# Kernel tuning notes

Hardware: AMD Instinct MI355X
Metric: run time of the kernel (lower is better)

The kernel has to match this reference:

```python
import jax, jax.numpy as jnp
import numpy as np

N = 20000      # num nodes
E = 320000     # num edges (avg degree 16)
F_IN = 518     # object_feature_dim
D = 128        # node_embedding_dim (= GAT out_channels)
ED = 32        # edge_embedding_dim
R = 26         # num_relations
H = 4          # GAT heads (concat=False -> mean over heads)
HID = 256      # node_encoder hidden


def _gat_layer(x, src, dst, ea, lin, lin_e, att_s, att_d, att_e, bias):
    """PyG GATConv: add_self_loops=True (fill_value='mean'), concat=False, negative_slope=0.2."""
    n = x.shape[0]
    ones = jnp.ones((src.shape[0],), x.dtype)
    cnt = jax.ops.segment_sum(ones, dst, num_segments=n)                    # [N]
    loop_ea = jax.ops.segment_sum(ea, dst, num_segments=n) / jnp.maximum(cnt, 1.0)[:, None]
    idx = jnp.arange(n)
    s = jnp.concatenate([src, idx])
    d = jnp.concatenate([dst, idx])
    ea2 = jnp.concatenate([ea, loop_ea], axis=0)                            # [E+N, ED]
    h = (x @ lin).reshape(n, H, D)                                          # [N,H,D]
    a_s = jnp.einsum('nhd,hd->nh', h, att_s)                                # [N,H]
    a_d = jnp.einsum('nhd,hd->nh', h, att_d)
    e = (ea2 @ lin_e).reshape(-1, H, D)                                     # [E+N,H,D]
    a_e = jnp.einsum('ehd,hd->eh', e, att_e)
    alpha = jax.nn.leaky_relu(a_s[s] + a_d[d] + a_e, 0.2)                   # [E+N,H]
    amax = jax.ops.segment_max(alpha, d, num_segments=n)
    alpha = jnp.exp(alpha - amax[d])
    denom = jax.ops.segment_sum(alpha, d, num_segments=n)
    alpha = alpha / (denom[d] + 1e-16)                                      # segment softmax
    msg = h[s] * alpha[:, :, None]                                          # [E+N,H,D]
    out = jax.ops.segment_sum(msg, d, num_segments=n)                       # [N,H,D]
    return out.mean(axis=1) + bias                                          # concat=False


def setup_inputs() -> dict:
    key = jax.random.key(0)
    ks = jax.random.split(key, 18)
    g = lambda k, shp, s=0.05: jax.random.normal(k, shp, jnp.float32) * s
    return {
        'x': g(ks[0], (N, F_IN), 1.0),
        'edge_index': jax.random.randint(ks[1], (2, E), 0, N),
        'edge_type': jax.random.randint(ks[2], (E,), 0, R),
        'w1': g(ks[3], (F_IN, HID)), 'b1': jnp.zeros((HID,), jnp.float32),
        'w2': g(ks[4], (HID, D)),    'b2': jnp.zeros((D,), jnp.float32),
        'rel_emb': g(ks[5], (R, ED), 1.0),
        'lin1': g(ks[6], (D, H * D)), 'line1': g(ks[7], (ED, H * D)),
        'atts1': g(ks[8], (H, D)), 'attd1': g(ks[9], (H, D)), 'atte1': g(ks[10], (H, D)),
        'bias1': jnp.zeros((D,), jnp.float32),
        'lin2': g(ks[11], (D, H * D)), 'line2': g(ks[12], (ED, H * D)),
        'atts2': g(ks[13], (H, D)), 'attd2': g(ks[14], (H, D)), 'atte2': g(ks[15], (H, D)),
        'bias2': jnp.zeros((D,), jnp.float32),
    }


def reference(x, edge_index, edge_type, w1, b1, w2, b2, rel_emb,
              lin1, line1, atts1, attd1, atte1, bias1,
              lin2, line2, atts2, attd2, atte2, bias2):
    src, dst = edge_index[0], edge_index[1]
    # node encoder (dropout inactive in eval)
    h = jax.nn.relu(x @ w1 + b1) @ w2 + b2                                  # [N,D]
    ea = rel_emb[edge_type]                                                 # [E,ED]
    h = jax.nn.relu(_gat_layer(h, src, dst, ea, lin1, line1, atts1, attd1, atte1, bias1))
    h = jax.nn.relu(_gat_layer(h, src, dst, ea, lin2, line2, atts2, attd2, atte2, bias2))
    return h
```

## Files before the change

### kernel.cpp

```cpp
#include <hip/hip_runtime.h>
#include <math.h>

#define N_NODES 20000
#define MP      20032
#define N_EDGES 320000
#define F_IN    518
#define HIDDEN  256
#define DIM     128
#define NH      4

typedef __attribute__((ext_vector_type(8))) short bf16x8;
typedef __attribute__((ext_vector_type(4))) float f32x4;
typedef unsigned short ushort_t;

__device__ __forceinline__ float lrelu02(float x) { return x > 0.f ? x : 0.2f * x; }

__device__ __forceinline__ void gl_lds16(const void* g, void* l) {
    __builtin_amdgcn_global_load_lds(
        (const __attribute__((address_space(1))) unsigned int*)g,
        (__attribute__((address_space(3))) unsigned int*)l, 16, 0, 0);
}

__device__ __forceinline__ unsigned int hi16(float v) { return __float_as_uint(v) >> 16; }
__device__ __forceinline__ unsigned int lo16(float v) {
    unsigned int h = __float_as_uint(v) & 0xFFFF0000u;
    return __float_as_uint(v - __uint_as_float(h)) >> 16;
}
__device__ __forceinline__ unsigned int rnd16(float v) {
    unsigned int u = __float_as_uint(v);
    return (u + 0x7FFFu + ((u >> 16) & 1u)) >> 16;
}
__device__ __forceinline__ float bfl(unsigned int u) { return __uint_as_float(u << 16); }
__device__ __forceinline__ float bfh(unsigned int u) { return __uint_as_float(u & 0xFFFF0000u); }

__global__ __launch_bounds__(256, 4) void gemm_mfma_v2(
    const ushort_t* __restrict__ Ah, const ushort_t* __restrict__ Al,
    const ushort_t* __restrict__ Bh, const ushort_t* __restrict__ Bl,
    const float* __restrict__ bias,
    int M, int K8, int N, int act,
    float* __restrict__ Cf,
    ushort_t* __restrict__ Ch, ushort_t* __restrict__ Cl,
    ushort_t* __restrict__ Cb,
    ushort_t* __restrict__ Ca)
{
    __shared__ __align__(16) ushort_t lds[12288];
    const int tid = threadIdx.x;
    const int w = tid >> 6, lane = tid & 63;
    const int row0 = blockIdx.y * 64, col0 = blockIdx.x * 128;
    const int nkb = K8 >> 2;
    const int m16 = lane & 15, q = lane >> 4;
    const bool use_al = (Al != nullptr);

    f32x4 acc[4][2] = {};

    for (int kb = 0; kb < nkb; ++kb) {
        const size_t kc = (size_t)(kb * 4 + w);
        const size_t aoff = (kc * MP + row0) * 8 + lane * 8;
        const size_t boff = (kc * N + col0) * 8 + lane * 8;
        gl_lds16(Ah + aoff, &lds[w * 512]);
        if (use_al) gl_lds16(Al + aoff, &lds[2048 + w * 512]);
        gl_lds16(Bh + boff,       &lds[4096 + w * 1024]);
        gl_lds16(Bh + boff + 512, &lds[4096 + w * 1024 + 512]);
        gl_lds16(Bl + boff,       &lds[8192 + w * 1024]);
        gl_lds16(Bl + boff + 512, &lds[8192 + w * 1024 + 512]);
        __syncthreads();

        bf16x8 fah[4], fal[4], fbh[2], fbl[2];
        const int fa = q * 512 + m16 * 8;
        #pragma unroll
        for (int mi = 0; mi < 4; ++mi) {
            fah[mi] = *(const bf16x8*)&lds[fa + mi * 128];
            if (use_al) fal[mi] = *(const bf16x8*)&lds[2048 + fa + mi * 128];
        }
        const int fb = q * 1024 + (w * 32 + m16) * 8;
        #pragma unroll
        for (int ni = 0; ni < 2; ++ni) {
            fbh[ni] = *(const bf16x8*)&lds[4096 + fb + ni * 128];
            fbl[ni] = *(const bf16x8*)&lds[8192 + fb + ni * 128];
        }
        #pragma unroll
        for (int mi = 0; mi < 4; ++mi)
            #pragma unroll
            for (int ni = 0; ni < 2; ++ni) {
                acc[mi][ni] = __builtin_amdgcn_mfma_f32_16x16x32_bf16(fah[mi], fbh[ni], acc[mi][ni], 0, 0, 0);
                acc[mi][ni] = __builtin_amdgcn_mfma_f32_16x16x32_bf16(fah[mi], fbl[ni], acc[mi][ni], 0, 0, 0);
            }
        if (use_al) {
            #pragma unroll
            for (int mi = 0; mi < 4; ++mi)
                #pragma unroll
                for (int ni = 0; ni < 2; ++ni)
                    acc[mi][ni] = __builtin_amdgcn_mfma_f32_16x16x32_bf16(fal[mi], fbh[ni], acc[mi][ni], 0, 0, 0);
        }
        __syncthreads();
    }

    #pragma unroll
    for (int ni = 0; ni < 2; ++ni) {
        const int col = col0 + w * 32 + ni * 16 + m16;
        const float bb = bias ? bias[col] : 0.f;
        #pragma unroll
        for (int mi = 0; mi < 4; ++mi) {
            #pragma unroll
            for (int r = 0; r < 4; ++r) {
                const int row = row0 + mi * 16 + q * 4 + r;
                if (row < M) {
                    float v = acc[mi][ni][r] + bb;
                    if (act) v = fmaxf(v, 0.f);
                    if (Cf) Cf[(size_t)row * N + col] = v;
                    if (Cb) Cb[(size_t)row * N + col] = (ushort_t)rnd16(v);
                    const size_t p = (((size_t)(col >> 3)) * MP + row) * 8 + (col & 7);
                    if (Ch) { Ch[p] = (ushort_t)hi16(v); Cl[p] = (ushort_t)lo16(v); }
                    if (Ca) Ca[p] = (ushort_t)rnd16(v);
                }
            }
        }
    }
}

__global__ __launch_bounds__(256) void conv_a_t_kernel(
    const float* __restrict__ x, ushort_t* __restrict__ xh, ushort_t* __restrict__ xl)
{
    __shared__ float tile[64][68];
    const int tid = threadIdx.x;
    const int r0 = blockIdx.x * 64;
    const int c0 = blockIdx.y * 64;

    #pragma unroll
    for (int it = 0; it < 4; ++it) {
        const int r = (tid >> 4) + it * 16;
        const int c = (tid & 15) * 4;
        const int gr = r0 + r, gc = c0 + c;
        float4 v = {0.f, 0.f, 0.f, 0.f};
        if (gr < N_NODES) {
            if (gc + 3 < F_IN) {
                v = *(const float4*)(x + (size_t)gr * F_IN + gc);
            } else {
                float tmp[4] = {0.f, 0.f, 0.f, 0.f};
                #pragma unroll
                for (int u = 0; u < 4; ++u)
                    if (gc + u < F_IN) tmp[u] = x[(size_t)gr * F_IN + gc + u];
                v.x = tmp[0]; v.y = tmp[1]; v.z = tmp[2]; v.w = tmp[3];
            }
        }
        tile[r][c] = v.x; tile[r][c+1] = v.y; tile[r][c+2] = v.z; tile[r][c+3] = v.w;
    }
    __syncthreads();

    const int k8l = tid >> 5;
    const int k8 = (c0 >> 3) + k8l;
    if (k8 >= 68) return;
    const int rr = (tid & 31) * 2;
    #pragma unroll
    for (int u = 0; u < 2; ++u) {
        const int r = rr + u;
        unsigned int hp[4], lp[4];
        #pragma unroll
        for (int i = 0; i < 4; ++i) {
            const float v0 = tile[r][k8l * 8 + 2 * i];
            const float v1 = tile[r][k8l * 8 + 2 * i + 1];
            hp[i] = (hi16(v1) << 16) | hi16(v0);
            lp[i] = (lo16(v1) << 16) | lo16(v0);
        }
        const size_t p = ((size_t)k8 * MP + r0 + r) * 8;
        *(uint4*)(xh + p) = make_uint4(hp[0], hp[1], hp[2], hp[3]);
        *(uint4*)(xl + p) = make_uint4(lp[0], lp[1], lp[2], lp[3]);
    }
}

#define W1_T (68 * 256 * 8)
#define W2_T (32 * 128 * 8)
#define L_T  (16 * 512 * 8)
__global__ __launch_bounds__(256) void conv_w_all_kernel(
    const float* __restrict__ w1, const float* __restrict__ w2,
    const float* __restrict__ l0, const float* __restrict__ l1,
    ushort_t* __restrict__ w1h, ushort_t* __restrict__ w1l,
    ushort_t* __restrict__ w2h, ushort_t* __restrict__ w2l,
    ushort_t* __restrict__ l0h, ushort_t* __restrict__ l0l,
    ushort_t* __restrict__ l1h, ushort_t* __restrict__ l1l)
{
    int idx = blockIdx.x * 256 + threadIdx.x;
    const float* w; ushort_t *bh, *bl; int K, N, local;
    if (idx < W1_T) { w = w1; bh = w1h; bl = w1l; K = F_IN; N = HIDDEN; local = idx; }
    else if (idx < W1_T + W2_T) { w = w2; bh = w2h; bl = w2l; K = HIDDEN; N = DIM; local = idx - W1_T; }
    else if (idx < W1_T + W2_T + L_T) { w = l0; bh = l0h; bl = l0l; K = DIM; N = 512; local = idx - W1_T - W2_T; }
    else if (idx < W1_T + W2_T + 2 * L_T) { w = l1; bh = l1h; bl = l1l; K = DIM; N = 512; local = idx - W1_T - W2_T - L_T; }
    else return;
    const int j = local & 7;
    const int rem = local >> 3;
    const int n = rem % N;
    const int k = (rem / N) * 8 + j;
    const float v = (k < K) ? w[(size_t)k * N + n] : 0.f;
    bh[local] = (ushort_t)hi16(v);
    bl[local] = (ushort_t)lo16(v);
}

__global__ __launch_bounds__(256) void wa2_kernel(
    const float* __restrict__ lin0, const float* __restrict__ lin1,
    const float* __restrict__ atts0, const float* __restrict__ attd0,
    const float* __restrict__ atts1, const float* __restrict__ attd1,
    float* __restrict__ wa_s0, float* __restrict__ wa_d0,
    float* __restrict__ wa_s1, float* __restrict__ wa_d1)
{
    const int wrk = blockIdx.x * 256 + threadIdx.x;
    if (wrk >= 2048) return;
    const int L = wrk >> 10;
    const int sd = (wrk >> 9) & 1;
    const int p = wrk & 511;
    const int h = p >> 7, d = p & 127;
    const float* lin = L ? lin1 : lin0;
    const float* av = L ? (sd ? attd1 : atts1) : (sd ? attd0 : atts0);
    float* out = L ? (sd ? wa_d1 : wa_s1) : (sd ? wa_d0 : wa_s0);
    const float* lp = lin + (size_t)d * (NH * DIM) + h * DIM;
    const float* ap = av + h * DIM;
    float acc = 0.f;
    #pragma unroll 8
    for (int i = 0; i < DIM; ++i) acc += lp[i] * ap[i];
    out[h * DIM + d] = acc;
}

__global__ __launch_bounds__(256) void as_ad_kernel(
    const float* __restrict__ xb, const float* __restrict__ wa_s,
    const float* __restrict__ wa_d, float* __restrict__ a_s, float* __restrict__ a_d)
{
    const int gw = blockIdx.x * 4 + (threadIdx.x >> 6);
    const int lane = threadIdx.x & 63;
    if (gw >= N_NODES * NH) return;
    const int n = gw >> 2, h = gw & 3;
    const float* hp = xb + (size_t)n * DIM;
    float2 hv = *(const float2*)(hp + lane * 2);
    float2 sv = *(const float2*)(wa_s + h * DIM + lane * 2);
    float2 dv = *(const float2*)(wa_d + h * DIM + lane * 2);
    float s = hv.x * sv.x + hv.y * sv.y;
    float d = hv.x * dv.x + hv.y * dv.y;
    #pragma unroll
    for (int off = 32; off > 0; off >>= 1) {
        s += __shfl_down(s, off);
        d += __shfl_down(d, off);
    }
    if (lane == 0) { a_s[n * 4 + h] = s; a_d[n * 4 + h] = d; }
}

__global__ __launch_bounds__(128) void rel_table2_kernel(
    const float* __restrict__ rel_emb,
    const float* __restrict__ line0, const float* __restrict__ atte0,
    const float* __restrict__ line1, const float* __restrict__ atte1,
    float* __restrict__ table)
{
    __shared__ float we[32][NH];
    const int L = blockIdx.x;
    const float* line = L ? line1 : line0;
    const float* atte = L ? atte1 : atte0;
    float* tab = table + L * 128;
    const int tid = threadIdx.x;
    const int k = tid >> 2, h = tid & 3;
    float acc = 0.f;
    for (int d = 0; d < DIM; ++d)
        acc += line[(size_t)k * (NH * DIM) + h * DIM + d] * atte[h * DIM + d];
    we[k][h] = acc;
    __syncthreads();
    if (tid < 26 * NH) {
        int r = tid >> 2, hh = tid & 3;
        float t = 0.f;
        for (int kk = 0; kk < 32; ++kk) t += rel_emb[r * 32 + kk] * we[kk][hh];
        tab[r * 4 + hh] = t;
    }
}

__global__ __launch_bounds__(256) void hist_kernel(
    const int* __restrict__ dst, int* __restrict__ cnt)
{
    const int e = blockIdx.x * blockDim.x + threadIdx.x;
    if (e >= N_EDGES) return;
    atomicAdd(&cnt[dst[e]], 1);
}

__global__ __launch_bounds__(1024) void scan_kernel(
    const int* __restrict__ cnt, int* __restrict__ ptr, int* __restrict__ ptr_copy)
{
    __shared__ int tsum[1024];
    const int tid = threadIdx.x;
    const int CH = 20;
    const int base = tid * CH;
    int s = 0;
    #pragma unroll
    for (int i = 0; i < CH; ++i) {
        int idx = base + i;
        if (idx < N_NODES) s += cnt[idx];
    }
    tsum[tid] = s;
    __syncthreads();
    for (int off = 1; off < 1024; off <<= 1) {
        int v = (tid >= off) ? tsum[tid - off] : 0;
        __syncthreads();
        tsum[tid] += v;
        __syncthreads();
    }
    int run = (tid == 0) ? 0 : tsum[tid - 1];
    #pragma unroll
    for (int i = 0; i < CH; ++i) {
        int idx = base + i;
        if (idx < N_NODES) {
            ptr[idx] = run;
            ptr_copy[idx] = run;
            run += cnt[idx];
        }
    }
    if (tid == 0) ptr[N_NODES] = N_EDGES;
}

__global__ __launch_bounds__(256) void scatter_kernel(
    const int* __restrict__ src, const int* __restrict__ dst, const int* __restrict__ etype,
    int* __restrict__ ptr_copy, int2* __restrict__ se)
{
    const int e = blockIdx.x * blockDim.x + threadIdx.x;
    if (e >= N_EDGES) return;
    const int d = dst[e];
    const int pos = atomicAdd(&ptr_copy[d], 1);
    se[pos] = make_int2(src[e], etype[e]);
}

__device__ __forceinline__ void agg_loop(
    int beg, int end, int n, int head, int cbase,
    const int2* __restrict__ se, const float* __restrict__ a_s, float adh,
    const float* __restrict__ table, const ushort_t* __restrict__ hb,
    float acc[8], float& dh, float& eh)
{
    int j = beg;
    for (; j + 2 <= end; j += 2) {
        const int2 E0 = se[j], E1 = se[j + 1];
        const uint4 g0 = *(const uint4*)(hb + (size_t)E0.x * 512 + cbase);
        const uint4 g1 = *(const uint4*)(hb + (size_t)E1.x * 512 + cbase);
        const float a0 = a_s[E0.x * 4 + head];
        const float t0 = table[E0.y * 4 + head];
        const float a1 = a_s[E1.x * 4 + head];
        const float t1 = table[E1.y * 4 + head];
        const float p0 = __expf(lrelu02(a0 + adh + t0));
        const float p1 = __expf(lrelu02(a1 + adh + t1));
        eh += t0 + t1;
        dh += p0 + p1;
        acc[0] += p0 * bfl(g0.x) + p1 * bfl(g1.x);
        acc[1] += p0 * bfh(g0.x) + p1 * bfh(g1.x);
        acc[2] += p0 * bfl(g0.y) + p1 * bfl(g1.y);
        acc[3] += p0 * bfh(g0.y) + p1 * bfh(g1.y);
        acc[4] += p0 * bfl(g0.z) + p1 * bfl(g1.z);
        acc[5] += p0 * bfh(g0.z) + p1 * bfh(g1.z);
        acc[6] += p0 * bfl(g0.w) + p1 * bfl(g1.w);
        acc[7] += p0 * bfh(g0.w) + p1 * bfh(g1.w);
    }
    if (j < end) {
        const int2 E0 = se[j];
        const uint4 g0 = *(const uint4*)(hb + (size_t)E0.x * 512 + cbase);
        const float a0 = a_s[E0.x * 4 + head];
        const float t0 = table[E0.y * 4 + head];
        const float p0 = __expf(lrelu02(a0 + adh + t0));
        eh += t0; dh += p0;
        acc[0] += p0 * bfl(g0.x); acc[1] += p0 * bfh(g0.x);
        acc[2] += p0 * bfl(g0.y); acc[3] += p0 * bfh(g0.y);
        acc[4] += p0 * bfl(g0.z); acc[5] += p0 * bfh(g0.z);
        acc[6] += p0 * bfl(g0.w); acc[7] += p0 * bfh(g0.w);
    }
    const float inv = 1.0f / fmaxf((float)(end - beg), 1.0f);
    const float ps = __expf(lrelu02(a_s[n * 4 + head] + adh + eh * inv));
    dh += ps;
    const uint4 gs = *(const uint4*)(hb + (size_t)n * 512 + cbase);
    acc[0] += ps * bfl(gs.x); acc[1] += ps * bfh(gs.x);
    acc[2] += ps * bfl(gs.y); acc[3] += ps * bfh(gs.y);
    acc[4] += ps * bfl(gs.z); acc[5] += ps * bfh(gs.z);
    acc[6] += ps * bfl(gs.w); acc[7] += ps * bfh(gs.w);
}

__global__ __launch_bounds__(256) void node_agg_f_kernel(
    const int* __restrict__ ptr, const int2* __restrict__ se,
    const float* __restrict__ a_s, const float* __restrict__ a_d,
    const float* __restrict__ table, const ushort_t* __restrict__ hb,
    const float* __restrict__ bias, ushort_t* __restrict__ oa,
    const float* __restrict__ wa_s2, const float* __restrict__ wa_d2,
    float* __restrict__ a_s2, float* __restrict__ a_d2)
{
    const int n = blockIdx.x * 4 + (threadIdx.x >> 6);
    const int lane = threadIdx.x & 63;
    if (n >= N_NODES) return;
    const int beg = ptr[n], end = ptr[n + 1];
    const int head = lane >> 4;
    const int cbase = lane * 8;
    const float adh = a_d[n * 4 + head];

    float acc[8] = {};
    float dh = 0.f, eh = 0.f;
    agg_loop(beg, end, n, head, cbase, se, a_s, adh, table, hb, acc, dh, eh);

    const float ih = 0.25f / (dh + 1e-16f);
    float t[8];
    #pragma unroll
    for (int k = 0; k < 8; ++k) {
        t[k] = acc[k] * ih;
        t[k] += __shfl_xor(t[k], 16);
        t[k] += __shfl_xor(t[k], 32);
    }
    if (lane < 16) {
        const float4 b0 = *(const float4*)(bias + cbase);
        const float4 b1 = *(const float4*)(bias + cbase + 4);
        float o[8];
        o[0] = fmaxf(t[0] + b0.x, 0.f); o[1] = fmaxf(t[1] + b0.y, 0.f);
        o[2] = fmaxf(t[2] + b0.z, 0.f); o[3] = fmaxf(t[3] + b0.w, 0.f);
        o[4] = fmaxf(t[4] + b1.x, 0.f); o[5] = fmaxf(t[5] + b1.y, 0.f);
        o[6] = fmaxf(t[6] + b1.z, 0.f); o[7] = fmaxf(t[7] + b1.w, 0.f);
        unsigned int up[4];
        #pragma unroll
        for (int i = 0; i < 4; ++i)
            up[i] = (rnd16(o[2*i+1]) << 16) | rnd16(o[2*i]);
        *(uint4*)(oa + ((size_t)lane * MP + n) * 8) = make_uint4(up[0], up[1], up[2], up[3]);
        float pss[4] = {0,0,0,0}, pdd[4] = {0,0,0,0};
        #pragma unroll
        for (int h = 0; h < NH; ++h) {
            const float* ws = wa_s2 + h * DIM + cbase;
            const float* wd = wa_d2 + h * DIM + cbase;
            #pragma unroll
            for (int i = 0; i < 8; ++i) {
                pss[h] += o[i] * ws[i];
                pdd[h] += o[i] * wd[i];
            }
        }
        #pragma unroll
        for (int m = 1; m < 16; m <<= 1) {
            #pragma unroll
            for (int h = 0; h < NH; ++h) {
                pss[h] += __shfl_xor(pss[h], m);
                pdd[h] += __shfl_xor(pdd[h], m);
            }
        }
        if (lane == 0) {
            float4 vs = {pss[0], pss[1], pss[2], pss[3]};
            float4 vd = {pdd[0], pdd[1], pdd[2], pdd[3]};
            *(float4*)(a_s2 + n * 4) = vs;
            *(float4*)(a_d2 + n * 4) = vd;
        }
    }
}

__global__ __launch_bounds__(256) void node_agg_s_kernel(
    const int* __restrict__ ptr, const int2* __restrict__ se,
    const float* __restrict__ a_s, const float* __restrict__ a_d,
    const float* __restrict__ table, const ushort_t* __restrict__ hb,
    const float* __restrict__ bias, float* __restrict__ outf)
{
    const int n = blockIdx.x * 4 + (threadIdx.x >> 6);
    const int lane = threadIdx.x & 63;
    if (n >= N_NODES) return;
    const int beg = ptr[n], end = ptr[n + 1];
    const int head = lane >> 4;
    const int cbase = lane * 8;
    const float adh = a_d[n * 4 + head];

    float acc[8] = {};
    float dh = 0.f, eh = 0.f;
    agg_loop(beg, end, n, head, cbase, se, a_s, adh, table, hb, acc, dh, eh);

    const float ih = 0.25f / (dh + 1e-16f);
    float t[8];
    #pragma unroll
    for (int k = 0; k < 8; ++k) {
        t[k] = acc[k] * ih;
        t[k] += __shfl_xor(t[k], 16);
        t[k] += __shfl_xor(t[k], 32);
    }
    if (lane < 16) {
        const float4 b0 = *(const float4*)(bias + cbase);
        const float4 b1 = *(const float4*)(bias + cbase + 4);
        float4 v0, v1;
        v0.x = fmaxf(t[0] + b0.x, 0.f); v0.y = fmaxf(t[1] + b0.y, 0.f);
        v0.z = fmaxf(t[2] + b0.z, 0.f); v0.w = fmaxf(t[3] + b0.w, 0.f);
        v1.x = fmaxf(t[4] + b1.x, 0.f); v1.y = fmaxf(t[5] + b1.y, 0.f);
        v1.z = fmaxf(t[6] + b1.z, 0.f); v1.w = fmaxf(t[7] + b1.w, 0.f);
        *(float4*)(outf + (size_t)n * DIM + cbase) = v0;
        *(float4*)(outf + (size_t)n * DIM + cbase + 4) = v1;
    }
}

extern "C" void kernel_launch(void* const* d_in, const int* in_sizes, int n_in,
                              void* d_out, int out_size, void* d_ws, size_t ws_size,
                              hipStream_t stream)
{
    const float* x       = (const float*)d_in[0];
    const int*   eidx    = (const int*)d_in[1];
    const int*   etype   = (const int*)d_in[2];
    const float* w1      = (const float*)d_in[3];
    const float* b1      = (const float*)d_in[4];
    const float* w2      = (const float*)d_in[5];
    const float* b2      = (const float*)d_in[6];
    const float* rel_emb = (const float*)d_in[7];
    const float* lin[2]  = {(const float*)d_in[8],  (const float*)d_in[14]};
    const float* line[2] = {(const float*)d_in[9],  (const float*)d_in[15]};
    const float* atts[2] = {(const float*)d_in[10], (const float*)d_in[16]};
    const float* attd[2] = {(const float*)d_in[11], (const float*)d_in[17]};
    const float* atte[2] = {(const float*)d_in[12], (const float*)d_in[18]};
    const float* bias[2] = {(const float*)d_in[13], (const float*)d_in[19]};
    const int* src = eidx;
    const int* dst = eidx + N_EDGES;

    char* base = (char*)d_ws;
    size_t off = 0;
    auto alloc = [&](size_t bytes) -> void* {
        void* p = base + off;
        off = (off + bytes + 255) & ~(size_t)255;
        return p;
    };
    ushort_t* xh  = (ushort_t*)alloc((size_t)68 * MP * 8 * 2);
    ushort_t* xl  = (ushort_t*)alloc((size_t)68 * MP * 8 * 2);
    ushort_t* h1h = (ushort_t*)alloc((size_t)32 * MP * 8 * 2);
    ushort_t* h1l = (ushort_t*)alloc((size_t)32 * MP * 8 * 2);
    ushort_t* x0a = (ushort_t*)alloc((size_t)16 * MP * 8 * 2);
    void* reg1    = alloc((size_t)16 * MP * 8 * 4);
    ushort_t* w1h = (ushort_t*)alloc(W1_T * 2);
    ushort_t* w1l = (ushort_t*)alloc(W1_T * 2);
    ushort_t* w2h = (ushort_t*)alloc(W2_T * 2);
    ushort_t* w2l = (ushort_t*)alloc(W2_T * 2);
    ushort_t* l0h = (ushort_t*)alloc(L_T * 2);
    ushort_t* l0l = (ushort_t*)alloc(L_T * 2);
    ushort_t* l1h = (ushort_t*)alloc(L_T * 2);
    ushort_t* l1l = (ushort_t*)alloc(L_T * 2);
    float* a_s0  = (float*)alloc(N_NODES * 4 * 4);
    float* a_d0  = (float*)alloc(N_NODES * 4 * 4);
    float* a_s1  = (float*)alloc(N_NODES * 4 * 4);
    float* a_d1  = (float*)alloc(N_NODES * 4 * 4);
    float* table = (float*)alloc(2 * 128 * 4);
    float* wa_s0 = (float*)alloc(512 * 4);
    float* wa_d0 = (float*)alloc(512 * 4);
    float* wa_s1 = (float*)alloc(512 * 4);
    float* wa_d1 = (float*)alloc(512 * 4);
    int*  cnt_i  = (int*)alloc(N_NODES * 4);
    int*  ptr    = (int*)alloc((N_NODES + 4) * 4);
    int*  ptrc   = (int*)alloc(N_NODES * 4);
    int2* se     = (int2*)alloc((size_t)N_EDGES * 8);

    ushort_t* hb = xh;
    float* xbuf0 = (float*)reg1;
    ushort_t* x1a = (ushort_t*)reg1;

    const int mtiles = MP / 64;

    conv_a_t_kernel<<<dim3(MP / 64, 9), 256, 0, stream>>>(x, xh, xl);
    conv_w_all_kernel<<<(W1_T + W2_T + 2 * L_T + 255) / 256, 256, 0, stream>>>(
        w1, w2, lin[0], lin[1], w1h, w1l, w2h, w2l, l0h, l0l, l1h, l1l);
    wa2_kernel<<<8, 256, 0, stream>>>(lin[0], lin[1], atts[0], attd[0], atts[1], attd[1],
                                      wa_s0, wa_d0, wa_s1, wa_d1);
    rel_table2_kernel<<<2, 128, 0, stream>>>(rel_emb, line[0], atte[0], line[1], atte[1], table);

    hipMemsetAsync(cnt_i, 0, N_NODES * sizeof(int), stream);
    hist_kernel<<<(N_EDGES + 255) / 256, 256, 0, stream>>>(dst, cnt_i);
    scan_kernel<<<1, 1024, 0, stream>>>(cnt_i, ptr, ptrc);
    scatter_kernel<<<(N_EDGES + 255) / 256, 256, 0, stream>>>(src, dst, etype, ptrc, se);

    gemm_mfma_v2<<<dim3(HIDDEN / 128, mtiles), 256, 0, stream>>>(
        xh, xl, w1h, w1l, b1, N_NODES, 68, HIDDEN, 1, nullptr, h1h, h1l, nullptr, nullptr);
    gemm_mfma_v2<<<dim3(DIM / 128, mtiles), 256, 0, stream>>>(
        h1h, h1l, w2h, w2l, b2, N_NODES, 32, DIM, 0, xbuf0, nullptr, nullptr, nullptr, x0a);

    gemm_mfma_v2<<<dim3((NH * DIM) / 128, mtiles), 256, 0, stream>>>(
        x0a, nullptr, l0h, l0l, nullptr, N_NODES, 16, NH * DIM, 0, nullptr, nullptr, nullptr, hb, nullptr);
    as_ad_kernel<<<N_NODES, 256, 0, stream>>>(xbuf0, wa_s0, wa_d0, a_s0, a_d0);
    node_agg_f_kernel<<<(N_NODES + 3) / 4, 256, 0, stream>>>(
        ptr, se, a_s0, a_d0, table, hb, bias[0], x1a,
        wa_s1, wa_d1, a_s1, a_d1);

    gemm_mfma_v2<<<dim3((NH * DIM) / 128, mtiles), 256, 0, stream>>>(
        x1a, nullptr, l1h, l1l, nullptr, N_NODES, 16, NH * DIM, 0, nullptr, nullptr, nullptr, hb, nullptr);
    node_agg_s_kernel<<<(N_NODES + 3) / 4, 256, 0, stream>>>(
        ptr, se, a_s1, a_d1, table + 128, hb, bias[1], (float*)d_out);
}
```

Baseline: 418.5 us.

## Precompute per-edge attention exponentials in a separate kernel before aggregation

Adds an edge/self-loop kernel that computes exp(leaky_relu(a_s+a_d+table)) for all four heads per edge and per self-loop, writing them in CSR order through a recorded scatter position. The aggregation kernels then read these precomputed weights instead of recomputing them in each of the 16 lanes per head. The inner loop is also unrolled to four edges. This removes redundant exp and gather work inside the aggregation, at the cost of an extra kernel launch per layer, extra p4/pose/sp buffer traffic, and a serial per-node loop for the self-loop mean.

```diff
diff --git a/kernel.cpp b/kernel.cpp
--- a/kernel.cpp
+++ b/kernel.cpp
@@ -311,69 +311,112 @@
 
 __global__ __launch_bounds__(256) void scatter_kernel(
     const int* __restrict__ src, const int* __restrict__ dst, const int* __restrict__ etype,
-    int* __restrict__ ptr_copy, int2* __restrict__ se)
+    int* __restrict__ ptr_copy, int2* __restrict__ se, int* __restrict__ pose)
 {
     const int e = blockIdx.x * blockDim.x + threadIdx.x;
     if (e >= N_EDGES) return;
     const int d = dst[e];
     const int pos = atomicAdd(&ptr_copy[d], 1);
     se[pos] = make_int2(src[e], etype[e]);
+    pose[e] = pos;
+}
+
+#define EP_EBLK (N_EDGES / 256)
+__global__ __launch_bounds__(256) void edge_self_p_kernel(
+    const int* __restrict__ src, const int* __restrict__ dst, const int* __restrict__ etype,
+    const int* __restrict__ pose, const int* __restrict__ ptr, const int2* __restrict__ se,
+    const float* __restrict__ a_s, const float* __restrict__ a_d,
+    const float* __restrict__ table, float* __restrict__ p4, float* __restrict__ sp)
+{
+    const int b = blockIdx.x;
+    if (b < EP_EBLK) {
+        const int e = b * 256 + threadIdx.x;
+        const int s = src[e], d = dst[e], et = etype[e];
+        const float4 as = *(const float4*)(a_s + s * 4);
+        const float4 ad = *(const float4*)(a_d + d * 4);
+        const float4 t  = *(const float4*)(table + et * 4);
+        float4 o;
+        o.x = __expf(lrelu02(as.x + ad.x + t.x));
+        o.y = __expf(lrelu02(as.y + ad.y + t.y));
+        o.z = __expf(lrelu02(as.z + ad.z + t.z));
+        o.w = __expf(lrelu02(as.w + ad.w + t.w));
+        *(float4*)(p4 + (size_t)pose[e] * 4) = o;
+    } else {
+        const int n = (b - EP_EBLK) * 256 + threadIdx.x;
+        if (n >= N_NODES) return;
+        const int beg = ptr[n], end = ptr[n + 1];
+        float t0 = 0.f, t1 = 0.f, t2 = 0.f, t3 = 0.f;
+        for (int j = beg; j < end; ++j) {
+            const float4 t = *(const float4*)(table + se[j].y * 4);
+            t0 += t.x; t1 += t.y; t2 += t.z; t3 += t.w;
+        }
+        const float inv = 1.0f / fmaxf((float)(end - beg), 1.0f);
+        const float4 as = *(const float4*)(a_s + n * 4);
+        const float4 ad = *(const float4*)(a_d + n * 4);
+        float4 o;
+        o.x = __expf(lrelu02(as.x + ad.x + t0 * inv));
+        o.y = __expf(lrelu02(as.y + ad.y + t1 * inv));
+        o.z = __expf(lrelu02(as.z + ad.z + t2 * inv));
+        o.w = __expf(lrelu02(as.w + ad.w + t3 * inv));
+        *(float4*)(sp + n * 4) = o;
+    }
+}
+
+__device__ __forceinline__ void acc8(float acc[8], float p, const uint4 g)
+{
+    acc[0] += p * bfl(g.x); acc[1] += p * bfh(g.x);
+    acc[2] += p * bfl(g.y); acc[3] += p * bfh(g.y);
+    acc[4] += p * bfl(g.z); acc[5] += p * bfh(g.z);
+    acc[6] += p * bfl(g.w); acc[7] += p * bfh(g.w);
 }
 
 __device__ __forceinline__ void agg_loop(
     int beg, int end, int n, int head, int cbase,
-    const int2* __restrict__ se, const float* __restrict__ a_s, float adh,
-    const float* __restrict__ table, const ushort_t* __restrict__ hb,
-    float acc[8], float& dh, float& eh)
-{
+    const int2* __restrict__ se, const float* __restrict__ p4,
+    const float* __restrict__ sp, const ushort_t* __restrict__ hb,
+    float acc[8], float& dh)
+{
+    const uint4 gs = *(const uint4*)(hb + (size_t)n * 512 + cbase);
+    const float ps = sp[n * 4 + head];
+
     int j = beg;
+    for (; j + 4 <= end; j += 4) {
+        const int2 e0 = se[j],     e1 = se[j + 1];
+        const int2 e2 = se[j + 2], e3 = se[j + 3];
+        const float* pj = p4 + ((size_t)j * 4 + head);
+        const float p0 = pj[0], p1 = pj[4], p2 = pj[8], p3 = pj[12];
+        const uint4 g0 = *(const uint4*)(hb + (size_t)e0.x * 512 + cbase);
+        const uint4 g1 = *(const uint4*)(hb + (size_t)e1.x * 512 + cbase);
+        const uint4 g2 = *(const uint4*)(hb + (size_t)e2.x * 512 + cbase);
+        const uint4 g3 = *(const uint4*)(hb + (size_t)e3.x * 512 + cbase);
+        dh += (p0 + p1) + (p2 + p3);
+        acc8(acc, p0, g0); acc8(acc, p1, g1);
+        acc8(acc, p2, g2); acc8(acc, p3, g3);
+    }
     for (; j + 2 <= end; j += 2) {
-        const int2 E0 = se[j], E1 = se[j + 1];
-        const uint4 g0 = *(const uint4*)(hb + (size_t)E0.x * 512 + cbase);
-        const uint4 g1 = *(const uint4*)(hb + (size_t)E1.x * 512 + cbase);
-        const float a0 = a_s[E0.x * 4 + head];
-        const float t0 = table[E0.y * 4 + head];
-        const float a1 = a_s[E1.x * 4 + head];
-        const float t1 = table[E1.y * 4 + head];
-        const float p0 = __expf(lrelu02(a0 + adh + t0));
-        const float p1 = __expf(lrelu02(a1 + adh + t1));
-        eh += t0 + t1;
+        const int2 e0 = se[j], e1 = se[j + 1];
+        const float* pj = p4 + ((size_t)j * 4 + head);
+        const float p0 = pj[0], p1 = pj[4];
+        const uint4 g0 = *(const uint4*)(hb + (size_t)e0.x * 512 + cbase);
+        const uint4 g1 = *(const uint4*)(hb + (size_t)e1.x * 512 + cbase);
         dh += p0 + p1;
-        acc[0] += p0 * bfl(g0.x) + p1 * bfl(g1.x);
-        acc[1] += p0 * bfh(g0.x) + p1 * bfh(g1.x);
-        acc[2] += p0 * bfl(g0.y) + p1 * bfl(g1.y);
-        acc[3] += p0 * bfh(g0.y) + p1 * bfh(g1.y);
-        acc[4] += p0 * bfl(g0.z) + p1 * bfl(g1.z);
-        acc[5] += p0 * bfh(g0.z) + p1 * bfh(g1.z);
-        acc[6] += p0 * bfl(g0.w) + p1 * bfl(g1.w);
-        acc[7] += p0 * bfh(g0.w) + p1 * bfh(g1.w);
+        acc8(acc, p0, g0); acc8(acc, p1, g1);
     }
     if (j < end) {
-        const int2 E0 = se[j];
-        const uint4 g0 = *(const uint4*)(hb + (size_t)E0.x * 512 + cbase);
-        const float a0 = a_s[E0.x * 4 + head];
-        const float t0 = table[E0.y * 4 + head];
-        const float p0 = __expf(lrelu02(a0 + adh + t0));
-        eh += t0; dh += p0;
-        acc[0] += p0 * bfl(g0.x); acc[1] += p0 * bfh(g0.x);
-        acc[2] += p0 * bfl(g0.y); acc[3] += p0 * bfh(g0.y);
-        acc[4] += p0 * bfl(g0.z); acc[5] += p0 * bfh(g0.z);
-        acc[6] += p0 * bfl(g0.w); acc[7] += p0 * bfh(g0.w);
-    }
-    const float inv = 1.0f / fmaxf((float)(end - beg), 1.0f);
-    const float ps = __expf(lrelu02(a_s[n * 4 + head] + adh + eh * inv));
+        const int2 e0 = se[j];
+        const float p0 = p4[(size_t)j * 4 + head];
+        const uint4 g0 = *(const uint4*)(hb + (size_t)e0.x * 512 + cbase);
+        dh += p0;
+        acc8(acc, p0, g0);
+    }
     dh += ps;
-    const uint4 gs = *(const uint4*)(hb + (size_t)n * 512 + cbase);
-    acc[0] += ps * bfl(gs.x); acc[1] += ps * bfh(gs.x);
-    acc[2] += ps * bfl(gs.y); acc[3] += ps * bfh(gs.y);
-    acc[4] += ps * bfl(gs.z); acc[5] += ps * bfh(gs.z);
-    acc[6] += ps * bfl(gs.w); acc[7] += ps * bfh(gs.w);
+    acc8(acc, ps, gs);
 }
 
 __global__ __launch_bounds__(256) void node_agg_f_kernel(
     const int* __restrict__ ptr, const int2* __restrict__ se,
-    const float* __restrict__ a_s, const float* __restrict__ a_d,
-    const float* __restrict__ table, const ushort_t* __restrict__ hb,
+    const float* __restrict__ p4, const float* __restrict__ sp,
+    const ushort_t* __restrict__ hb,
     const float* __restrict__ bias, ushort_t* __restrict__ oa,
     const float* __restrict__ wa_s2, const float* __restrict__ wa_d2,
     float* __restrict__ a_s2, float* __restrict__ a_d2)
@@ -384,11 +427,10 @@
     const int beg = ptr[n], end = ptr[n + 1];
     const int head = lane >> 4;
     const int cbase = lane * 8;
-    const float adh = a_d[n * 4 + head];
 
     float acc[8] = {};
-    float dh = 0.f, eh = 0.f;
-    agg_loop(beg, end, n, head, cbase, se, a_s, adh, table, hb, acc, dh, eh);
+    float dh = 0.f;
+    agg_loop(beg, end, n, head, cbase, se, p4, sp, hb, acc, dh);
 
     const float ih = 0.25f / (dh + 1e-16f);
     float t[8];
@@ -441,8 +483,8 @@
 
 __global__ __launch_bounds__(256) void node_agg_s_kernel(
     const int* __restrict__ ptr, const int2* __restrict__ se,
-    const float* __restrict__ a_s, const float* __restrict__ a_d,
-    const float* __restrict__ table, const ushort_t* __restrict__ hb,
+    const float* __restrict__ p4, const float* __restrict__ sp,
+    const ushort_t* __restrict__ hb,
     const float* __restrict__ bias, float* __restrict__ outf)
 {
     const int n = blockIdx.x * 4 + (threadIdx.x >> 6);
@@ -451,11 +493,10 @@
     const int beg = ptr[n], end = ptr[n + 1];
     const int head = lane >> 4;
     const int cbase = lane * 8;
-    const float adh = a_d[n * 4 + head];
 
     float acc[8] = {};
-    float dh = 0.f, eh = 0.f;
-    agg_loop(beg, end, n, head, cbase, se, a_s, adh, table, hb, acc, dh, eh);
+    float dh = 0.f;
+    agg_loop(beg, end, n, head, cbase, se, p4, sp, hb, acc, dh);
 
     const float ih = 0.25f / (dh + 1e-16f);
     float t[8];
@@ -533,12 +574,16 @@
     int*  ptr    = (int*)alloc((N_NODES + 4) * 4);
     int*  ptrc   = (int*)alloc(N_NODES * 4);
     int2* se     = (int2*)alloc((size_t)N_EDGES * 8);
+    int*  pose   = (int*)alloc((size_t)N_EDGES * 4);
+    float* p4    = (float*)alloc((size_t)N_EDGES * 4 * 4);
+    float* sp    = (float*)alloc((size_t)N_NODES * 4 * 4);
 
     ushort_t* hb = xh;
     float* xbuf0 = (float*)reg1;
     ushort_t* x1a = (ushort_t*)reg1;
 
     const int mtiles = MP / 64;
+    const int ep_grid = EP_EBLK + (N_NODES + 255) / 256;
 
     conv_a_t_kernel<<<dim3(MP / 64, 9), 256, 0, stream>>>(x, xh, xl);
     conv_w_all_kernel<<<(W1_T + W2_T + 2 * L_T + 255) / 256, 256, 0, stream>>>(
@@ -550,7 +595,7 @@
     hipMemsetAsync(cnt_i, 0, N_NODES * sizeof(int), stream);
     hist_kernel<<<(N_EDGES + 255) / 256, 256, 0, stream>>>(dst, cnt_i);
     scan_kernel<<<1, 1024, 0, stream>>>(cnt_i, ptr, ptrc);
-    scatter_kernel<<<(N_EDGES + 255) / 256, 256, 0, stream>>>(src, dst, etype, ptrc, se);
+    scatter_kernel<<<(N_EDGES + 255) / 256, 256, 0, stream>>>(src, dst, etype, ptrc, se, pose);
 
     gemm_mfma_v2<<<dim3(HIDDEN / 128, mtiles), 256, 0, stream>>>(
         xh, xl, w1h, w1l, b1, N_NODES, 68, HIDDEN, 1, nullptr, h1h, h1l, nullptr, nullptr);
@@ -560,12 +605,16 @@
     gemm_mfma_v2<<<dim3((NH * DIM) / 128, mtiles), 256, 0, stream>>>(
         x0a, nullptr, l0h, l0l, nullptr, N_NODES, 16, NH * DIM, 0, nullptr, nullptr, nullptr, hb, nullptr);
     as_ad_kernel<<<N_NODES, 256, 0, stream>>>(xbuf0, wa_s0, wa_d0, a_s0, a_d0);
+    edge_self_p_kernel<<<ep_grid, 256, 0, stream>>>(
+        src, dst, etype, pose, ptr, se, a_s0, a_d0, table, p4, sp);
     node_agg_f_kernel<<<(N_NODES + 3) / 4, 256, 0, stream>>>(
-        ptr, se, a_s0, a_d0, table, hb, bias[0], x1a,
+        ptr, se, p4, sp, hb, bias[0], x1a,
         wa_s1, wa_d1, a_s1, a_d1);
 
     gemm_mfma_v2<<<dim3((NH * DIM) / 128, mtiles), 256, 0, stream>>>(
         x1a, nullptr, l1h, l1l, nullptr, N_NODES, 16, NH * DIM, 0, nullptr, nullptr, nullptr, hb, nullptr);
+    edge_self_p_kernel<<<ep_grid, 256, 0, stream>>>(
+        src, dst, etype, pose, ptr, se, a_s1, a_d1, table + 128, p4, sp);
     node_agg_s_kernel<<<(N_NODES + 3) / 4, 256, 0, stream>>>(
-        ptr, se, a_s1, a_d1, table + 128, hb, bias[1], (float*)d_out);
-}
+        ptr, se, p4, sp, hb, bias[1], (float*)d_out);
+}
```

Result: slower. 436.3 us (+4.2%).
